# Optimization experiments

Hardware: AMD Instinct MI355X
Metric: run time of the kernel (lower is better)

Reference implementation:

```python
import jax, jax.numpy as jnp
import numpy as np

DIM = 1024
N_HEADS = 16
HEAD_DIM = DIM // N_HEADS
MLP_RATIO = 4
LN_EPS = 1e-5


def _layer_norm(x, w):
    xf = x.astype(jnp.float32)
    mu = jnp.mean(xf, axis=-1, keepdims=True)
    var = jnp.var(xf, axis=-1, keepdims=True)
    y = (xf - mu) / jnp.sqrt(var + LN_EPS)
    return y * w[None, None, :]


def _apply_rope(x, cos, sin):
    # x: (b, s, h, d); cos, sin: (s, d/2)
    c = jnp.concatenate([cos, cos], axis=-1)[None, :, None, :]  # (1,s,1,d)
    s_ = jnp.concatenate([sin, sin], axis=-1)[None, :, None, :]
    x1, x2 = jnp.split(x, 2, axis=-1)
    rot = jnp.concatenate([-x2, x1], axis=-1)
    return x * c + rot * s_


def setup_inputs() -> dict:
    key = jax.random.key(0)
    ks = jax.random.split(key, 12)
    b, s = 2, 2048
    x = jax.random.normal(ks[0], (b, s, DIM), dtype=jnp.float32)
    rot_cos = jax.random.uniform(ks[1], (1, s, 1, 1, HEAD_DIM), dtype=jnp.float32)
    rot_sin = jax.random.uniform(ks[2], (1, s, 1, 1, HEAD_DIM), dtype=jnp.float32)
    w_init = 0.02
    params = {
        'ln1_w': jnp.ones((DIM,), jnp.float32),
        'w_qkv': jax.random.normal(ks[3], (3 * DIM, DIM), jnp.float32) * w_init,
        'w_out': jax.random.normal(ks[4], (DIM, DIM), jnp.float32) * w_init,
        'ln2_w': jnp.ones((DIM,), jnp.float32),
        'w_mlp1': jax.random.normal(ks[5], (MLP_RATIO * DIM, DIM), jnp.float32) * w_init,
        'b_mlp1': jnp.zeros((MLP_RATIO * DIM,), jnp.float32),
        'w_mlp2': jax.random.normal(ks[6], (DIM, MLP_RATIO * DIM), jnp.float32) * w_init,
        'b_mlp2': jnp.zeros((DIM,), jnp.float32),
    }
    return {'x': x, 'rot_cos': rot_cos, 'rot_sin': rot_sin, **params}


def reference(x, rot_cos, rot_sin, ln1_w, w_qkv, w_out, ln2_w, w_mlp1, b_mlp1, w_mlp2, b_mlp2):
    b, s, _ = x.shape
    # _split_rotary: (1,s,1,1,hd) -> (s, hd/2)
    cos = rot_cos[0, :, 0, 0, : HEAD_DIM // 2]
    sin = rot_sin[0, :, 0, 0, : HEAD_DIM // 2]

    x_skip = x
    h1 = _layer_norm(x, ln1_w)
    qkv = jnp.einsum('bsd,ed->bse', h1, w_qkv).reshape(b, s, 3, N_HEADS, HEAD_DIM)
    q, k, v = qkv[:, :, 0], qkv[:, :, 1], qkv[:, :, 2]
    q = _apply_rope(q, cos, sin)
    k = _apply_rope(k, cos, sin)

    # causal SDPA, scale = 1/sqrt(head_dim) (flex_attention default)
    scale = 1.0 / np.sqrt(HEAD_DIM)
    scores = jnp.einsum('bqhd,bkhd->bhqk', q, k) * scale
    causal = jnp.tril(jnp.ones((s, s), dtype=bool))
    scores = jnp.where(causal[None, None], scores, -jnp.inf)
    attn = jax.nn.softmax(scores, axis=-1)
    o = jnp.einsum('bhqk,bkhd->bqhd', attn, v).reshape(b, s, DIM)

    # attn out + residual (eval: dropout off, scale=1)
    x = x_skip + jnp.einsum('bsd,ed->bse', o, w_out)

    # MLP with tanh GELU + residual
    h2 = _layer_norm(x, ln2_w)
    u = jnp.einsum('bsd,ed->bse', h2, w_mlp1) + b_mlp1
    u = jax.nn.gelu(u, approximate=True)
    m = jnp.einsum('bse,de->bsd', u, w_mlp2) + b_mlp2
    return x + m
```

## Files before the change

kernel.cpp:

```cpp
#include <hip/hip_runtime.h>
#include <hip/hip_bf16.h>
#include <math.h>


#define B_ 2
#define S_ 2048
#define D_ 1024
#define H_ 16
#define DH_ 64
#define MLP_ 4096
#define ROWS_ (B_ * S_)

typedef short bf16x8 __attribute__((ext_vector_type(8)));
typedef float f32x4 __attribute__((ext_vector_type(4)));
typedef unsigned short ushort_t;
typedef ushort_t u16x4 __attribute__((ext_vector_type(4)));
typedef unsigned int u32x2 __attribute__((ext_vector_type(2)));

__device__ __forceinline__ float wave_reduce_sum(float v) {
  #pragma unroll
  for (int off = 32; off > 0; off >>= 1) v += __shfl_down(v, off, 64);
  return v;
}

__device__ __forceinline__ ushort_t f2bf(float v) {
  __hip_bfloat16 h = __float2bfloat16(v);
  return *(ushort_t*)&h;
}
__device__ __forceinline__ float bf2f(ushort_t u) {
  unsigned int v = ((unsigned int)u) << 16;
  union { unsigned int i; float f; } c; c.i = v; return c.f;
}

__device__ __forceinline__ void async_copy16(const void* g, void* l) {
  __builtin_amdgcn_global_load_lds(
      (const __attribute__((address_space(1))) void*)g,
      (__attribute__((address_space(3))) void*)l, 16, 0, 0);
}

__global__ __launch_bounds__(256) void cast_w_kernel(
    const float* __restrict__ s0, ushort_t* __restrict__ d0, int n0,
    const float* __restrict__ s1, ushort_t* __restrict__ d1, int n1,
    const float* __restrict__ s2, ushort_t* __restrict__ d2, int n2,
    const float* __restrict__ s3, ushort_t* __restrict__ d3, int n3) {
  const float* s; ushort_t* d; int n;
  switch (blockIdx.y) {
    case 0: s = s0; d = d0; n = n0; break;
    case 1: s = s1; d = d1; n = n1; break;
    case 2: s = s2; d = d2; n = n2; break;
    default: s = s3; d = d3; n = n3; break;
  }
  const int i = (blockIdx.x * 256 + threadIdx.x) * 4;
  if (i < n) {
    const float4 v = *reinterpret_cast<const float4*>(s + i);
    u16x4 o;
    o[0] = f2bf(v.x); o[1] = f2bf(v.y); o[2] = f2bf(v.z); o[3] = f2bf(v.w);
    *reinterpret_cast<u16x4*>(d + i) = o;
  }
}

__global__ __launch_bounds__(256) void ln_kernel(
    const float* __restrict__ x, const float* __restrict__ w,
    ushort_t* __restrict__ y) {
  const int row = blockIdx.x;
  const float4 v = reinterpret_cast<const float4*>(x + (size_t)row * D_)[threadIdx.x];
  float s  = v.x + v.y + v.z + v.w;
  float ss = v.x * v.x + v.y * v.y + v.z * v.z + v.w * v.w;
  __shared__ float red[8];
  const int wave = threadIdx.x >> 6, lane = threadIdx.x & 63;
  const float ws1 = wave_reduce_sum(s);
  const float ws2 = wave_reduce_sum(ss);
  if (lane == 0) { red[wave] = ws1; red[4 + wave] = ws2; }
  __syncthreads();
  const float tot  = red[0] + red[1] + red[2] + red[3];
  const float tot2 = red[4] + red[5] + red[6] + red[7];
  const float mu  = tot * (1.0f / D_);
  const float var = tot2 * (1.0f / D_) - mu * mu;
  const float inv = rsqrtf(var + 1e-5f);
  const float4 wv = reinterpret_cast<const float4*>(w)[threadIdx.x];
  u16x4 o;
  o[0] = f2bf((v.x - mu) * inv * wv.x);
  o[1] = f2bf((v.y - mu) * inv * wv.y);
  o[2] = f2bf((v.z - mu) * inv * wv.z);
  o[3] = f2bf((v.w - mu) * inv * wv.w);
  reinterpret_cast<u16x4*>(y + (size_t)row * D_)[threadIdx.x] = o;
}

__device__ __forceinline__ float gelu_tanh(float u) {
  const float u3 = u * u * u;
  const float t = tanhf(0.7978845608028654f * (u + 0.044715f * u3));
  return 0.5f * u * (1.0f + t);
}

template <int FUSE, int OUTBF, int QKV>
__global__ __launch_bounds__(256) void gemm_bt(
    const ushort_t* __restrict__ A, const ushort_t* __restrict__ W,
    const float* __restrict__ bias, const float* __restrict__ res,
    void* __restrict__ Cv, ushort_t* __restrict__ VtOut,
    int M, int N, int K, int sm, int sn, int rects_n) {
  __shared__ ushort_t As[2][128 * 32];
  __shared__ ushort_t Bs[2][128 * 32];
  const int tid = threadIdx.x;
  const int wave = tid >> 6, lane = tid & 63;
  const int l15 = lane & 15, quad = lane >> 4;

  const int lin = blockIdx.x;
  const int xcd = lin & 7, j = lin >> 3;
  const int rm = xcd / rects_n, rn = xcd % rects_n;
  const int m0 = (rm * sm + (j % sm)) * 128;
  const int n0 = (rn * sn + (j / sm)) * 128;
  const int wm = (wave & 1) * 64, wn = (wave >> 1) * 64;

  const int srow = tid >> 2;
  const int gcol = (((tid & 3) ^ (srow & 3)) * 8);
  const ushort_t* Ag = A + (size_t)(m0 + srow) * K + gcol;
  const ushort_t* Wg = W + (size_t)(n0 + srow) * K + gcol;

  f32x4 acc[4][4] = {};
  const int rslot = (quad ^ (l15 & 3)) * 8;

  const int NI = K >> 5;
  async_copy16(Ag,          &As[0][tid * 8]);
  async_copy16(Ag + 64 * K, &As[0][2048 + tid * 8]);
  async_copy16(Wg,          &Bs[0][tid * 8]);
  async_copy16(Wg + 64 * K, &Bs[0][2048 + tid * 8]);

  for (int i = 0; i < NI; ++i) {
    const int st = i & 1;
    __syncthreads();
    if (i + 1 < NI) {
      const int k1 = (i + 1) << 5;
      async_copy16(Ag + k1,          &As[1 - st][tid * 8]);
      async_copy16(Ag + 64 * K + k1, &As[1 - st][2048 + tid * 8]);
      async_copy16(Wg + k1,          &Bs[1 - st][tid * 8]);
      async_copy16(Wg + 64 * K + k1, &Bs[1 - st][2048 + tid * 8]);
    }
    bf16x8 af[4], bfr[4];
    #pragma unroll
    for (int ii = 0; ii < 4; ++ii) {
      af[ii]  = *(const bf16x8*)&As[st][(wm + ii * 16 + l15) * 32 + rslot];
      bfr[ii] = *(const bf16x8*)&Bs[st][(wn + ii * 16 + l15) * 32 + rslot];
    }
    #pragma unroll
    for (int ii = 0; ii < 4; ++ii)
      #pragma unroll
      for (int jj = 0; jj < 4; ++jj)
        acc[ii][jj] = __builtin_amdgcn_mfma_f32_16x16x32_bf16(af[ii], bfr[jj], acc[ii][jj], 0, 0, 0);
  }

  #pragma unroll
  for (int i = 0; i < 4; ++i) {
    const int mb = m0 + wm + i * 16 + quad * 4;
    #pragma unroll
    for (int jj = 0; jj < 4; ++jj) {
      const int n = n0 + wn + jj * 16 + l15;
      float cv[4];
      #pragma unroll
      for (int r = 0; r < 4; ++r) {
        float c = acc[i][jj][r];
        if (FUSE & 1) c += bias[n];
        if (FUSE & 2) c = gelu_tanh(c);
        if (FUSE & 4) c += res[(size_t)(mb + r) * N + n];
        cv[r] = c;
      }
      if (QKV && ((n0 + wn) >> 10) == 2) {
        const int d  = n & 63;
        const int hh = (n >> 6) & 15;
        const int bb = mb >> 11;
        const int ss = mb & (S_ - 1);
        u16x4 pk;
        #pragma unroll
        for (int r = 0; r < 4; ++r) pk[r] = f2bf(cv[r]);
        *(u16x4*)&VtOut[((size_t)(bb * H_ + hh) * DH_ + d) * S_ + ss] = pk;
      } else {
        #pragma unroll
        for (int r = 0; r < 4; ++r) {
          if (OUTBF) ((ushort_t*)Cv)[(size_t)(mb + r) * N + n] = f2bf(cv[r]);
          else       ((float*)Cv)[(size_t)(mb + r) * N + n]   = cv[r];
        }
      }
    }
  }
}

template <int FUSE, int OUTBF>
__global__ __launch_bounds__(256) void gemm64_bt(
    const ushort_t* __restrict__ A, const ushort_t* __restrict__ W,
    const float* __restrict__ bias, const float* __restrict__ res,
    void* __restrict__ Cv, int M, int N, int K, int sm, int sn, int rects_n) {
  __shared__ ushort_t As[2][64 * 64];
  __shared__ ushort_t Bs[2][128 * 64];
  const int tid = threadIdx.x;
  const int wave = tid >> 6, lane = tid & 63;
  const int l15 = lane & 15, quad = lane >> 4;

  const int lin = blockIdx.x;
  const int xcd = lin & 7, j = lin >> 3;
  const int rm = xcd / rects_n, rn = xcd % rects_n;
  const int m0 = (rm * sm + (j % sm)) * 64;
  const int n0 = (rn * sn + (j / sm)) * 128;
  const int wn = wave * 32;

  const int srow = tid >> 3;
  const int gcol = (((tid & 7) ^ (srow & 7)) * 8);
  const ushort_t* Ag = A + (size_t)(m0 + srow) * K + gcol;
  const ushort_t* Wg = W + (size_t)(n0 + srow) * K + gcol;

  f32x4 acc[4][2] = {};

  const int NI = K >> 6;
  #pragma unroll
  for (int i = 0; i < 2; ++i)
    async_copy16(Ag + (size_t)i * 32 * K, &As[0][i * 2048 + tid * 8]);
  #pragma unroll
  for (int i = 0; i < 4; ++i)
    async_copy16(Wg + (size_t)i * 32 * K, &Bs[0][i * 2048 + tid * 8]);

  for (int it = 0; it < NI; ++it) {
    const int st = it & 1;
    __syncthreads();
    if (it + 1 < NI) {
      const int k1 = (it + 1) << 6;
      #pragma unroll
      for (int i = 0; i < 2; ++i)
        async_copy16(Ag + (size_t)i * 32 * K + k1, &As[1 - st][i * 2048 + tid * 8]);
      #pragma unroll
      for (int i = 0; i < 4; ++i)
        async_copy16(Wg + (size_t)i * 32 * K + k1, &Bs[1 - st][i * 2048 + tid * 8]);
    }
    #pragma unroll
    for (int kk = 0; kk < 2; ++kk) {
      const int slot = (((kk * 4 + quad) ^ (l15 & 7)) * 8);
      bf16x8 af[4], bfr[2];
      #pragma unroll
      for (int i = 0; i < 4; ++i)
        af[i] = *(const bf16x8*)&As[st][(i * 16 + l15) * 64 + slot];
      #pragma unroll
      for (int jj = 0; jj < 2; ++jj)
        bfr[jj] = *(const bf16x8*)&Bs[st][(wn + jj * 16 + l15) * 64 + slot];
      #pragma unroll
      for (int i = 0; i < 4; ++i)
        #pragma unroll
        for (int jj = 0; jj < 2; ++jj)
          acc[i][jj] = __builtin_amdgcn_mfma_f32_16x16x32_bf16(af[i], bfr[jj], acc[i][jj], 0, 0, 0);
    }
  }

  #pragma unroll
  for (int i = 0; i < 4; ++i) {
    const int mb = m0 + i * 16 + quad * 4;
    #pragma unroll
    for (int jj = 0; jj < 2; ++jj) {
      const int n = n0 + wn + jj * 16 + l15;
      #pragma unroll
      for (int r = 0; r < 4; ++r) {
        float c = acc[i][jj][r];
        if (FUSE & 1) c += bias[n];
        if (FUSE & 2) c = gelu_tanh(c);
        if (FUSE & 4) c += res[(size_t)(mb + r) * N + n];
        if (OUTBF) ((ushort_t*)Cv)[(size_t)(mb + r) * N + n] = f2bf(c);
        else       ((float*)Cv)[(size_t)(mb + r) * N + n]   = c;
      }
    }
  }
}

__global__ __launch_bounds__(256) void rope_kernel(
    const ushort_t* __restrict__ qkv, const float* __restrict__ cosb,
    const float* __restrict__ sinb, ushort_t* __restrict__ Qo,
    ushort_t* __restrict__ Ko) {
  const int bs = blockIdx.x;
  const int s  = bs & (S_ - 1);
  const int b  = bs >> 11;
  const int t  = threadIdx.x;
  const ushort_t* base = qkv + (size_t)bs * (3 * D_);
  #pragma unroll
  for (int i = 0; i < 8; ++i) {
    const int e = i * 256 + t;
    const int which = e >> 10;
    const int rem = e & 1023;
    const int h = rem >> 6;
    const int d = rem & 63;
    const float val = bf2f(base[e]);
    float out;
    if (d < 32) {
      out = val * cosb[s * 64 + d] - bf2f(base[e + 32]) * sinb[s * 64 + d];
    } else {
      out = val * cosb[s * 64 + d - 32] + bf2f(base[e - 32]) * sinb[s * 64 + d - 32];
    }
    const size_t oidx = (((size_t)(b * H_ + h)) * S_ + s) * DH_ + d;
    if (which == 0) Qo[oidx] = f2bf(out * 0.125f);
    else            Ko[oidx] = f2bf(out);
  }
}

#define PPAD 72

__global__ __launch_bounds__(256) void attn_kernel(
    const ushort_t* __restrict__ Qb, const ushort_t* __restrict__ Kb,
    const ushort_t* __restrict__ Vt, ushort_t* __restrict__ O) {
  const int wave = threadIdx.x >> 6;
  const int lane = threadIdx.x & 63;
  const int l15 = lane & 15, quad = lane >> 4;
  const int bh = blockIdx.y;
  const int b = bh >> 4, h = bh & 15;
  const int wl = blockIdx.x * 4 + wave;
  const int g  = (wl & 1) ? (63 - (wl >> 1)) : (wl >> 1);
  const int q0 = g * 32;

  __shared__ ushort_t Plds[4][2][16 * PPAD];

  const ushort_t* Kbh = Kb + (size_t)bh * S_ * DH_;
  const ushort_t* Vbh = Vt + (size_t)bh * DH_ * S_;

  bf16x8 qb[2][2];
  #pragma unroll
  for (int t = 0; t < 2; ++t) {
    const ushort_t* qptr = Qb + ((size_t)bh * S_ + q0 + t * 16 + l15) * DH_ + quad * 8;
    qb[t][0] = *(const bf16x8*)(qptr);
    qb[t][1] = *(const bf16x8*)(qptr + 32);
  }

  f32x4 o_acc[2][4] = {};
  float m_run[2] = {-1e30f, -1e30f}, l_run[2] = {0.0f, 0.0f};

  const int nch = (q0 >> 6) + 1;

  bf16x8 ka[4][2];
  #pragma unroll
  for (int kt = 0; kt < 4; ++kt) {
    const ushort_t* kp = Kbh + (size_t)(kt * 16 + l15) * DH_ + quad * 8;
    ka[kt][0] = *(const bf16x8*)kp;
    ka[kt][1] = *(const bf16x8*)(kp + 32);
  }

  for (int c = 0; c < nch; ++c) {
    const int k0 = c << 6;

    bf16x8 va[4][2];
    #pragma unroll
    for (int mt = 0; mt < 4; ++mt) {
      const ushort_t* vp = Vbh + (size_t)(mt * 16 + l15) * S_ + k0 + quad * 8;
      va[mt][0] = *(const bf16x8*)vp;
      va[mt][1] = *(const bf16x8*)(vp + 32);
    }

    f32x4 st[2][4];
    #pragma unroll
    for (int t = 0; t < 2; ++t)
      #pragma unroll
      for (int kt = 0; kt < 4; ++kt) {
        f32x4 z = {0.0f, 0.0f, 0.0f, 0.0f};
        z = __builtin_amdgcn_mfma_f32_16x16x32_bf16(ka[kt][0], qb[t][0], z, 0, 0, 0);
        z = __builtin_amdgcn_mfma_f32_16x16x32_bf16(ka[kt][1], qb[t][1], z, 0, 0, 0);
        st[t][kt] = z;
      }

    if (c + 1 < nch) {
      const int k1 = (c + 1) << 6;
      bf16x8 kan[4][2];
      #pragma unroll
      for (int kt = 0; kt < 4; ++kt) {
        const ushort_t* kp = Kbh + (size_t)(k1 + kt * 16 + l15) * DH_ + quad * 8;
        kan[kt][0] = *(const bf16x8*)kp;
        kan[kt][1] = *(const bf16x8*)(kp + 32);
      }
      #pragma unroll
      for (int kt = 0; kt < 4; ++kt) { ka[kt][0] = kan[kt][0]; ka[kt][1] = kan[kt][1]; }
    }

    if (c == nch - 1) {
      #pragma unroll
      for (int t = 0; t < 2; ++t) {
        const int query = q0 + t * 16 + l15;
        #pragma unroll
        for (int kt = 0; kt < 4; ++kt)
          #pragma unroll
          for (int r = 0; r < 4; ++r)
            if (k0 + kt * 16 + quad * 4 + r > query) st[t][kt][r] = -1e30f;
      }
    }

    #pragma unroll
    for (int t = 0; t < 2; ++t) {
      float mx = -1e30f;
      #pragma unroll
      for (int kt = 0; kt < 4; ++kt)
        #pragma unroll
        for (int r = 0; r < 4; ++r) mx = fmaxf(mx, st[t][kt][r]);
      mx = fmaxf(mx, __shfl_xor(mx, 16, 64));
      mx = fmaxf(mx, __shfl_xor(mx, 32, 64));
      const float m_new = fmaxf(m_run[t], mx);
      const float alpha = __expf(m_run[t] - m_new);
      float rs = 0.0f;
      #pragma unroll
      for (int kt = 0; kt < 4; ++kt)
        #pragma unroll
        for (int r = 0; r < 4; ++r) {
          const float e = __expf(st[t][kt][r] - m_new);
          st[t][kt][r] = e;
          rs += e;
        }
      rs += __shfl_xor(rs, 16, 64);
      rs += __shfl_xor(rs, 32, 64);
      l_run[t] = l_run[t] * alpha + rs;
      m_run[t] = m_new;
      #pragma unroll
      for (int mt = 0; mt < 4; ++mt)
        #pragma unroll
        for (int r = 0; r < 4; ++r) o_acc[t][mt][r] *= alpha;
    }

    #pragma unroll
    for (int t = 0; t < 2; ++t) {
      ushort_t* Pw = &Plds[wave][t][0];
      #pragma unroll
      for (int kt = 0; kt < 4; ++kt) {
        u32x2 wpair;
        wpair[0] = (unsigned)f2bf(st[t][kt][0]) | ((unsigned)f2bf(st[t][kt][1]) << 16);
        wpair[1] = (unsigned)f2bf(st[t][kt][2]) | ((unsigned)f2bf(st[t][kt][3]) << 16);
        *(u32x2*)&Pw[l15 * PPAD + kt * 16 + quad * 4] = wpair;
      }
      asm volatile("s_waitcnt lgkmcnt(0)" ::: "memory");
      const bf16x8 pb0 = *(const bf16x8*)&Pw[l15 * PPAD + quad * 8];
      const bf16x8 pb1 = *(const bf16x8*)&Pw[l15 * PPAD + 32 + quad * 8];
      #pragma unroll
      for (int mt = 0; mt < 4; ++mt) {
        o_acc[t][mt] = __builtin_amdgcn_mfma_f32_16x16x32_bf16(va[mt][0], pb0, o_acc[t][mt], 0, 0, 0);
        o_acc[t][mt] = __builtin_amdgcn_mfma_f32_16x16x32_bf16(va[mt][1], pb1, o_acc[t][mt], 0, 0, 0);
      }
    }
  }

  #pragma unroll
  for (int t = 0; t < 2; ++t) {
    const float inv = 1.0f / l_run[t];
    #pragma unroll
    for (int mt = 0; mt < 4; ++mt) {
      u16x4 pk;
      #pragma unroll
      for (int r = 0; r < 4; ++r) pk[r] = f2bf(o_acc[t][mt][r] * inv);
      *(u16x4*)&O[(((size_t)b * S_ + q0 + t * 16 + l15) * H_ + h) * DH_ + mt * 16 + quad * 4] = pk;
    }
  }
}

extern "C" void kernel_launch(void* const* d_in, const int* in_sizes, int n_in,
                              void* d_out, int out_size, void* d_ws, size_t ws_size,
                              hipStream_t stream) {
  const float* x       = (const float*)d_in[0];
  const float* rot_cos = (const float*)d_in[1];
  const float* rot_sin = (const float*)d_in[2];
  const float* ln1_w   = (const float*)d_in[3];
  const float* w_qkv   = (const float*)d_in[4];
  const float* w_out   = (const float*)d_in[5];
  const float* ln2_w   = (const float*)d_in[6];
  const float* w_mlp1  = (const float*)d_in[7];
  const float* b_mlp1  = (const float*)d_in[8];
  const float* w_mlp2  = (const float*)d_in[9];
  const float* b_mlp2  = (const float*)d_in[10];
  float* out = (float*)d_out;

  char* wsb = (char*)d_ws;
  const size_t MB = 1u << 20;
  ushort_t* h1_bf  = (ushort_t*)(wsb + 0 * MB);
  ushort_t* qkv_bf = (ushort_t*)(wsb + 8 * MB);
  ushort_t* q_bf   = (ushort_t*)(wsb + 32 * MB);
  ushort_t* k_bf   = (ushort_t*)(wsb + 40 * MB);
  ushort_t* v_t    = (ushort_t*)(wsb + 48 * MB);
  ushort_t* o_bf   = (ushort_t*)(wsb + 56 * MB);
  float*    x2     = (float*)   (wsb + 64 * MB);
  ushort_t* u_bf   = (ushort_t*)(wsb + 80 * MB);
  ushort_t* wq_bf  = (ushort_t*)(wsb + 112 * MB);
  ushort_t* wo_bf  = (ushort_t*)(wsb + 118 * MB);
  ushort_t* w1_bf  = (ushort_t*)(wsb + 120 * MB);
  ushort_t* w2_bf  = (ushort_t*)(wsb + 128 * MB);
  (void)ws_size; (void)in_sizes; (void)n_in; (void)out_size;

  dim3 b256(256);

  cast_w_kernel<<<dim3(4096, 4), b256, 0, stream>>>(
      w_qkv, wq_bf, 3 * D_ * D_, w_out, wo_bf, D_ * D_,
      w_mlp1, w1_bf, MLP_ * D_, w_mlp2, w2_bf, MLP_ * D_);
  ln_kernel<<<dim3(ROWS_), b256, 0, stream>>>(x, ln1_w, h1_bf);
  gemm_bt<0, 1, 1><<<dim3(768), b256, 0, stream>>>(
      h1_bf, wq_bf, nullptr, nullptr, qkv_bf, v_t, ROWS_, 3 * D_, D_, 16, 6, 4);
  rope_kernel<<<dim3(ROWS_), b256, 0, stream>>>(qkv_bf, rot_cos, rot_sin, q_bf, k_bf);
  attn_kernel<<<dim3(16, B_ * H_), b256, 0, stream>>>(q_bf, k_bf, v_t, o_bf);
  gemm64_bt<4, 0><<<dim3(512), b256, 0, stream>>>(
      o_bf, wo_bf, nullptr, x, x2, ROWS_, D_, D_, 16, 4, 2);
  ln_kernel<<<dim3(ROWS_), b256, 0, stream>>>(x2, ln2_w, h1_bf);
  gemm_bt<3, 1, 0><<<dim3(1024), b256, 0, stream>>>(
      h1_bf, w1_bf, b_mlp1, nullptr, u_bf, nullptr, ROWS_, MLP_, D_, 16, 8, 4);
  gemm64_bt<5, 0><<<dim3(512), b256, 0, stream>>>(
      u_bf, w2_bf, b_mlp2, x2, out, ROWS_, D_, MLP_, 16, 4, 2);
}
```

Baseline: 386.6 us.

## Split attention waves to 16 queries, use exp2 softmax, retune GEMM LDS swizzle

Each attention wave now handles 16 query rows instead of 32, and the grid doubles so there are twice as many waves, which improves load balance across the causal triangle. The Q scale folds in log2(e) so softmax can use the hardware exp2 instruction instead of __expf. The GEMM LDS XOR swizzle now uses (row>>1)&3 to reduce bank conflicts. The tradeoff is that K/V loads are no longer shared across two query tiles per wave, so each K/V chunk is read twice as often.

```diff
diff --git a/kernel.cpp b/kernel.cpp
--- a/kernel.cpp
+++ b/kernel.cpp
@@ -30,6 +30,14 @@
 __device__ __forceinline__ float bf2f(ushort_t u) {
   unsigned int v = ((unsigned int)u) << 16;
   union { unsigned int i; float f; } c; c.i = v; return c.f;
+}
+
+__device__ __forceinline__ float exp2_fast(float x) {
+#if __has_builtin(__builtin_amdgcn_exp2f)
+  return __builtin_amdgcn_exp2f(x);
+#else
+  return exp2f(x);
+#endif
 }
 
 __device__ __forceinline__ void async_copy16(const void* g, void* l) {
@@ -112,12 +120,12 @@
   const int wm = (wave & 1) * 64, wn = (wave >> 1) * 64;
 
   const int srow = tid >> 2;
-  const int gcol = (((tid & 3) ^ (srow & 3)) * 8);
+  const int gcol = (((tid & 3) ^ ((srow >> 1) & 3)) * 8);
   const ushort_t* Ag = A + (size_t)(m0 + srow) * K + gcol;
   const ushort_t* Wg = W + (size_t)(n0 + srow) * K + gcol;
 
   f32x4 acc[4][4] = {};
-  const int rslot = (quad ^ (l15 & 3)) * 8;
+  const int rslot = (quad ^ ((l15 >> 1) & 3)) * 8;
 
   const int NI = K >> 5;
   async_copy16(Ag,          &As[0][tid * 8]);
@@ -289,7 +297,7 @@
       out = val * cosb[s * 64 + d - 32] + bf2f(base[e - 32]) * sinb[s * 64 + d - 32];
     }
     const size_t oidx = (((size_t)(b * H_ + h)) * S_ + s) * DH_ + d;
-    if (which == 0) Qo[oidx] = f2bf(out * 0.125f);
+    if (which == 0) Qo[oidx] = f2bf(out * 0.18033688736f);
     else            Ko[oidx] = f2bf(out);
   }
 }
@@ -305,24 +313,23 @@
   const int bh = blockIdx.y;
   const int b = bh >> 4, h = bh & 15;
   const int wl = blockIdx.x * 4 + wave;
-  const int g  = (wl & 1) ? (63 - (wl >> 1)) : (wl >> 1);
-  const int q0 = g * 32;
-
-  __shared__ ushort_t Plds[4][2][16 * PPAD];
+  const int g  = (wl & 1) ? (127 - (wl >> 1)) : (wl >> 1);
+  const int q0 = g * 16;
+
+  __shared__ ushort_t Plds[4][16 * PPAD];
 
   const ushort_t* Kbh = Kb + (size_t)bh * S_ * DH_;
   const ushort_t* Vbh = Vt + (size_t)bh * DH_ * S_;
 
-  bf16x8 qb[2][2];
-  #pragma unroll
-  for (int t = 0; t < 2; ++t) {
-    const ushort_t* qptr = Qb + ((size_t)bh * S_ + q0 + t * 16 + l15) * DH_ + quad * 8;
-    qb[t][0] = *(const bf16x8*)(qptr);
-    qb[t][1] = *(const bf16x8*)(qptr + 32);
-  }
-
-  f32x4 o_acc[2][4] = {};
-  float m_run[2] = {-1e30f, -1e30f}, l_run[2] = {0.0f, 0.0f};
+  bf16x8 qb[2];
+  {
+    const ushort_t* qptr = Qb + ((size_t)bh * S_ + q0 + l15) * DH_ + quad * 8;
+    qb[0] = *(const bf16x8*)(qptr);
+    qb[1] = *(const bf16x8*)(qptr + 32);
+  }
+
+  f32x4 o_acc[4] = {};
+  float m_run = -1e30f, l_run = 0.0f;
 
   const int nch = (q0 >> 6) + 1;
 
@@ -345,16 +352,14 @@
       va[mt][1] = *(const bf16x8*)(vp + 32);
     }
 
-    f32x4 st[2][4];
-    #pragma unroll
-    for (int t = 0; t < 2; ++t)
-      #pragma unroll
-      for (int kt = 0; kt < 4; ++kt) {
-        f32x4 z = {0.0f, 0.0f, 0.0f, 0.0f};
-        z = __builtin_amdgcn_mfma_f32_16x16x32_bf16(ka[kt][0], qb[t][0], z, 0, 0, 0);
-        z = __builtin_amdgcn_mfma_f32_16x16x32_bf16(ka[kt][1], qb[t][1], z, 0, 0, 0);
-        st[t][kt] = z;
-      }
+    f32x4 st[4];
+    #pragma unroll
+    for (int kt = 0; kt < 4; ++kt) {
+      f32x4 z = {0.0f, 0.0f, 0.0f, 0.0f};
+      z = __builtin_amdgcn_mfma_f32_16x16x32_bf16(ka[kt][0], qb[0], z, 0, 0, 0);
+      z = __builtin_amdgcn_mfma_f32_16x16x32_bf16(ka[kt][1], qb[1], z, 0, 0, 0);
+      st[kt] = z;
+    }
 
     if (c + 1 < nch) {
       const int k1 = (c + 1) << 6;
@@ -370,55 +375,50 @@
     }
 
     if (c == nch - 1) {
-      #pragma unroll
-      for (int t = 0; t < 2; ++t) {
-        const int query = q0 + t * 16 + l15;
-        #pragma unroll
-        for (int kt = 0; kt < 4; ++kt)
-          #pragma unroll
-          for (int r = 0; r < 4; ++r)
-            if (k0 + kt * 16 + quad * 4 + r > query) st[t][kt][r] = -1e30f;
-      }
-    }
-
-    #pragma unroll
-    for (int t = 0; t < 2; ++t) {
+      const int query = q0 + l15;
+      #pragma unroll
+      for (int kt = 0; kt < 4; ++kt)
+        #pragma unroll
+        for (int r = 0; r < 4; ++r)
+          if (k0 + kt * 16 + quad * 4 + r > query) st[kt][r] = -1e30f;
+    }
+
+    {
       float mx = -1e30f;
       #pragma unroll
       for (int kt = 0; kt < 4; ++kt)
         #pragma unroll
-        for (int r = 0; r < 4; ++r) mx = fmaxf(mx, st[t][kt][r]);
+        for (int r = 0; r < 4; ++r) mx = fmaxf(mx, st[kt][r]);
       mx = fmaxf(mx, __shfl_xor(mx, 16, 64));
       mx = fmaxf(mx, __shfl_xor(mx, 32, 64));
-      const float m_new = fmaxf(m_run[t], mx);
-      const float alpha = __expf(m_run[t] - m_new);
+      const float m_new = fmaxf(m_run, mx);
+      const float alpha = exp2_fast(m_run - m_new);
       float rs = 0.0f;
       #pragma unroll
       for (int kt = 0; kt < 4; ++kt)
         #pragma unroll
         for (int r = 0; r < 4; ++r) {
-          const float e = __expf(st[t][kt][r] - m_new);
-          st[t][kt][r] = e;
+          const float e = exp2_fast(st[kt][r] - m_new);
+          st[kt][r] = e;
           rs += e;
         }
       rs += __shfl_xor(rs, 16, 64);
       rs += __shfl_xor(rs, 32, 64);
-      l_run[t] = l_run[t] * alpha + rs;
-      m_run[t] = m_new;
+      l_run = l_run * alpha + rs;
+      m_run = m_new;
       #pragma unroll
       for (int mt = 0; mt < 4; ++mt)
         #pragma unroll
-        for (int r = 0; r < 4; ++r) o_acc[t][mt][r] *= alpha;
-    }
-
-    #pragma unroll
-    for (int t = 0; t < 2; ++t) {
-      ushort_t* Pw = &Plds[wave][t][0];
+        for (int r = 0; r < 4; ++r) o_acc[mt][r] *= alpha;
+    }
+
+    {
+      ushort_t* Pw = &Plds[wave][0];
       #pragma unroll
       for (int kt = 0; kt < 4; ++kt) {
         u32x2 wpair;
-        wpair[0] = (unsigned)f2bf(st[t][kt][0]) | ((unsigned)f2bf(st[t][kt][1]) << 16);
-        wpair[1] = (unsigned)f2bf(st[t][kt][2]) | ((unsigned)f2bf(st[t][kt][3]) << 16);
+        wpair[0] = (unsigned)f2bf(st[kt][0]) | ((unsigned)f2bf(st[kt][1]) << 16);
+        wpair[1] = (unsigned)f2bf(st[kt][2]) | ((unsigned)f2bf(st[kt][3]) << 16);
         *(u32x2*)&Pw[l15 * PPAD + kt * 16 + quad * 4] = wpair;
       }
       asm volatile("s_waitcnt lgkmcnt(0)" ::: "memory");
@@ -426,21 +426,20 @@
       const bf16x8 pb1 = *(const bf16x8*)&Pw[l15 * PPAD + 32 + quad * 8];
       #pragma unroll
       for (int mt = 0; mt < 4; ++mt) {
-        o_acc[t][mt] = __builtin_amdgcn_mfma_f32_16x16x32_bf16(va[mt][0], pb0, o_acc[t][mt], 0, 0, 0);
-        o_acc[t][mt] = __builtin_amdgcn_mfma_f32_16x16x32_bf16(va[mt][1], pb1, o_acc[t][mt], 0, 0, 0);
-      }
-    }
-  }
-
-  #pragma unroll
-  for (int t = 0; t < 2; ++t) {
-    const float inv = 1.0f / l_run[t];
+        o_acc[mt] = __builtin_amdgcn_mfma_f32_16x16x32_bf16(va[mt][0], pb0, o_acc[mt], 0, 0, 0);
+        o_acc[mt] = __builtin_amdgcn_mfma_f32_16x16x32_bf16(va[mt][1], pb1, o_acc[mt], 0, 0, 0);
+      }
+    }
+  }
+
+  {
+    const float inv = 1.0f / l_run;
     #pragma unroll
     for (int mt = 0; mt < 4; ++mt) {
       u16x4 pk;
       #pragma unroll
-      for (int r = 0; r < 4; ++r) pk[r] = f2bf(o_acc[t][mt][r] * inv);
-      *(u16x4*)&O[(((size_t)b * S_ + q0 + t * 16 + l15) * H_ + h) * DH_ + mt * 16 + quad * 4] = pk;
+      for (int r = 0; r < 4; ++r) pk[r] = f2bf(o_acc[mt][r] * inv);
+      *(u16x4*)&O[(((size_t)b * S_ + q0 + l15) * H_ + h) * DH_ + mt * 16 + quad * 4] = pk;
     }
   }
 }
@@ -486,7 +485,7 @@
   gemm_bt<0, 1, 1><<<dim3(768), b256, 0, stream>>>(
       h1_bf, wq_bf, nullptr, nullptr, qkv_bf, v_t, ROWS_, 3 * D_, D_, 16, 6, 4);
   rope_kernel<<<dim3(ROWS_), b256, 0, stream>>>(qkv_bf, rot_cos, rot_sin, q_bf, k_bf);
-  attn_kernel<<<dim3(16, B_ * H_), b256, 0, stream>>>(q_bf, k_bf, v_t, o_bf);
+  attn_kernel<<<dim3(32, B_ * H_), b256, 0, stream>>>(q_bf, k_bf, v_t, o_bf);
   gemm64_bt<4, 0><<<dim3(512), b256, 0, stream>>>(
       o_bf, wo_bf, nullptr, x, x2, ROWS_, D_, D_, 16, 4, 2);
   ln_kernel<<<dim3(ROWS_), b256, 0, stream>>>(x2, ln2_w, h1_bf);
```

Result: slower. 452.7 us (+17.1%).

## Split attention KV range across two waves with combine kernel, use exp2 softmax

Applied to the files above, without the earlier changes.

Each query tile's causal KV chunks are split into two halves processed by separate waves, which write unnormalized fp32 partial outputs plus running max and sum. A new combine kernel merges the two halves and writes bf16 output. The aim is more parallelism and better load balance for the attention stage. The change also folds log2(e) into the Q scale so softmax can use exp2, changes the GEMM LDS swizzle pattern, and adds s_setprio around the MFMA blocks. The cost is extra fp32 partial-output traffic and an additional kernel launch.

```diff
diff --git a/kernel.cpp b/kernel.cpp
--- a/kernel.cpp
+++ b/kernel.cpp
@@ -30,6 +30,14 @@
 __device__ __forceinline__ float bf2f(ushort_t u) {
   unsigned int v = ((unsigned int)u) << 16;
   union { unsigned int i; float f; } c; c.i = v; return c.f;
+}
+
+__device__ __forceinline__ float exp2_fast(float x) {
+#if __has_builtin(__builtin_amdgcn_exp2f)
+  return __builtin_amdgcn_exp2f(x);
+#else
+  return exp2f(x);
+#endif
 }
 
 __device__ __forceinline__ void async_copy16(const void* g, void* l) {
@@ -112,12 +120,12 @@
   const int wm = (wave & 1) * 64, wn = (wave >> 1) * 64;
 
   const int srow = tid >> 2;
-  const int gcol = (((tid & 3) ^ (srow & 3)) * 8);
+  const int gcol = (((tid & 3) ^ ((srow >> 1) & 3)) * 8);
   const ushort_t* Ag = A + (size_t)(m0 + srow) * K + gcol;
   const ushort_t* Wg = W + (size_t)(n0 + srow) * K + gcol;
 
   f32x4 acc[4][4] = {};
-  const int rslot = (quad ^ (l15 & 3)) * 8;
+  const int rslot = (quad ^ ((l15 >> 1) & 3)) * 8;
 
   const int NI = K >> 5;
   async_copy16(Ag,          &As[0][tid * 8]);
@@ -289,7 +297,7 @@
       out = val * cosb[s * 64 + d - 32] + bf2f(base[e - 32]) * sinb[s * 64 + d - 32];
     }
     const size_t oidx = (((size_t)(b * H_ + h)) * S_ + s) * DH_ + d;
-    if (which == 0) Qo[oidx] = f2bf(out * 0.125f);
+    if (which == 0) Qo[oidx] = f2bf(out * 0.18033688736f);
     else            Ko[oidx] = f2bf(out);
   }
 }
@@ -298,17 +306,43 @@
 
 __global__ __launch_bounds__(256) void attn_kernel(
     const ushort_t* __restrict__ Qb, const ushort_t* __restrict__ Kb,
-    const ushort_t* __restrict__ Vt, ushort_t* __restrict__ O) {
+    const ushort_t* __restrict__ Vt, float* __restrict__ Opart,
+    float2* __restrict__ MLpart) {
   const int wave = threadIdx.x >> 6;
   const int lane = threadIdx.x & 63;
   const int l15 = lane & 15, quad = lane >> 4;
   const int bh = blockIdx.y;
-  const int b = bh >> 4, h = bh & 15;
   const int wl = blockIdx.x * 4 + wave;
-  const int g  = (wl & 1) ? (63 - (wl >> 1)) : (wl >> 1);
+  const int j  = wl >> 1, half = wl & 1;
+  const int g  = (j & 1) ? (63 - (j >> 1)) : (j >> 1);
   const int q0 = g * 32;
 
   __shared__ ushort_t Plds[4][2][16 * PPAD];
+
+  const int nch   = (q0 >> 6) + 1;
+  const int c_mid = (nch + 1) >> 1;
+  const int c_lo  = half ? c_mid : 0;
+  const int c_hi  = half ? nch : c_mid;
+
+  float*  Obase  = Opart + (size_t)half * ((size_t)B_ * H_ * S_ * DH_)
+                 + ((size_t)bh * S_ + q0) * DH_;
+  float2* MLbase = MLpart + (size_t)half * ((size_t)B_ * H_ * S_)
+                 + (size_t)bh * S_ + q0;
+
+  if (c_lo >= c_hi) {
+    const f32x4 z = {0.0f, 0.0f, 0.0f, 0.0f};
+    #pragma unroll
+    for (int t = 0; t < 2; ++t)
+      #pragma unroll
+      for (int mt = 0; mt < 4; ++mt)
+        *(f32x4*)&Obase[(size_t)(t * 16 + l15) * DH_ + mt * 16 + quad * 4] = z;
+    if (quad == 0) {
+      #pragma unroll
+      for (int t = 0; t < 2; ++t)
+        MLbase[t * 16 + l15] = make_float2(-1e30f, 0.0f);
+    }
+    return;
+  }
 
   const ushort_t* Kbh = Kb + (size_t)bh * S_ * DH_;
   const ushort_t* Vbh = Vt + (size_t)bh * DH_ * S_;
@@ -324,17 +358,15 @@
   f32x4 o_acc[2][4] = {};
   float m_run[2] = {-1e30f, -1e30f}, l_run[2] = {0.0f, 0.0f};
 
-  const int nch = (q0 >> 6) + 1;
-
   bf16x8 ka[4][2];
   #pragma unroll
   for (int kt = 0; kt < 4; ++kt) {
-    const ushort_t* kp = Kbh + (size_t)(kt * 16 + l15) * DH_ + quad * 8;
+    const ushort_t* kp = Kbh + (size_t)(c_lo * 64 + kt * 16 + l15) * DH_ + quad * 8;
     ka[kt][0] = *(const bf16x8*)kp;
     ka[kt][1] = *(const bf16x8*)(kp + 32);
   }
 
-  for (int c = 0; c < nch; ++c) {
+  for (int c = c_lo; c < c_hi; ++c) {
     const int k0 = c << 6;
 
     bf16x8 va[4][2];
@@ -346,6 +378,7 @@
     }
 
     f32x4 st[2][4];
+    __builtin_amdgcn_s_setprio(1);
     #pragma unroll
     for (int t = 0; t < 2; ++t)
       #pragma unroll
@@ -355,8 +388,9 @@
         z = __builtin_amdgcn_mfma_f32_16x16x32_bf16(ka[kt][1], qb[t][1], z, 0, 0, 0);
         st[t][kt] = z;
       }
-
-    if (c + 1 < nch) {
+    __builtin_amdgcn_s_setprio(0);
+
+    if (c + 1 < c_hi) {
       const int k1 = (c + 1) << 6;
       bf16x8 kan[4][2];
       #pragma unroll
@@ -391,13 +425,13 @@
       mx = fmaxf(mx, __shfl_xor(mx, 16, 64));
       mx = fmaxf(mx, __shfl_xor(mx, 32, 64));
       const float m_new = fmaxf(m_run[t], mx);
-      const float alpha = __expf(m_run[t] - m_new);
+      const float alpha = exp2_fast(m_run[t] - m_new);
       float rs = 0.0f;
       #pragma unroll
       for (int kt = 0; kt < 4; ++kt)
         #pragma unroll
         for (int r = 0; r < 4; ++r) {
-          const float e = __expf(st[t][kt][r] - m_new);
+          const float e = exp2_fast(st[t][kt][r] - m_new);
           st[t][kt][r] = e;
           rs += e;
         }
@@ -424,25 +458,47 @@
       asm volatile("s_waitcnt lgkmcnt(0)" ::: "memory");
       const bf16x8 pb0 = *(const bf16x8*)&Pw[l15 * PPAD + quad * 8];
       const bf16x8 pb1 = *(const bf16x8*)&Pw[l15 * PPAD + 32 + quad * 8];
+      __builtin_amdgcn_s_setprio(1);
       #pragma unroll
       for (int mt = 0; mt < 4; ++mt) {
         o_acc[t][mt] = __builtin_amdgcn_mfma_f32_16x16x32_bf16(va[mt][0], pb0, o_acc[t][mt], 0, 0, 0);
         o_acc[t][mt] = __builtin_amdgcn_mfma_f32_16x16x32_bf16(va[mt][1], pb1, o_acc[t][mt], 0, 0, 0);
       }
+      __builtin_amdgcn_s_setprio(0);
     }
   }
 
   #pragma unroll
   for (int t = 0; t < 2; ++t) {
-    const float inv = 1.0f / l_run[t];
-    #pragma unroll
-    for (int mt = 0; mt < 4; ++mt) {
-      u16x4 pk;
-      #pragma unroll
-      for (int r = 0; r < 4; ++r) pk[r] = f2bf(o_acc[t][mt][r] * inv);
-      *(u16x4*)&O[(((size_t)b * S_ + q0 + t * 16 + l15) * H_ + h) * DH_ + mt * 16 + quad * 4] = pk;
-    }
-  }
+    #pragma unroll
+    for (int mt = 0; mt < 4; ++mt)
+      *(f32x4*)&Obase[(size_t)(t * 16 + l15) * DH_ + mt * 16 + quad * 4] = o_acc[t][mt];
+    if (quad == 0) MLbase[t * 16 + l15] = make_float2(m_run[t], l_run[t]);
+  }
+}
+
+__global__ __launch_bounds__(256) void attn_combine(
+    const float* __restrict__ Opart, const float2* __restrict__ MLpart,
+    ushort_t* __restrict__ O) {
+  const int tid = threadIdx.x;
+  const int row = blockIdx.x * 16 + (tid >> 4);
+  const int d0  = (tid & 15) * 4;
+  const size_t HALF_O  = (size_t)B_ * H_ * S_ * DH_;
+  const size_t HALF_ML = (size_t)B_ * H_ * S_;
+  const f32x4 o1 = *(const f32x4*)&Opart[(size_t)row * DH_ + d0];
+  const f32x4 o2 = *(const f32x4*)&Opart[HALF_O + (size_t)row * DH_ + d0];
+  const float2 ml1 = MLpart[row];
+  const float2 ml2 = MLpart[HALF_ML + row];
+  const float m  = fmaxf(ml1.x, ml2.x);
+  const float e1 = exp2_fast(ml1.x - m);
+  const float e2 = exp2_fast(ml2.x - m);
+  const float inv = 1.0f / (ml1.y * e1 + ml2.y * e2);
+  const int bh = row >> 11, q = row & (S_ - 1);
+  const int b = bh >> 4, h = bh & 15;
+  u16x4 pk;
+  #pragma unroll
+  for (int r = 0; r < 4; ++r) pk[r] = f2bf((o1[r] * e1 + o2[r] * e2) * inv);
+  *(u16x4*)&O[(((size_t)b * S_ + q) * H_ + h) * DH_ + d0] = pk;
 }
 
 extern "C" void kernel_launch(void* const* d_in, const int* in_sizes, int n_in,
@@ -471,10 +527,12 @@
   ushort_t* o_bf   = (ushort_t*)(wsb + 56 * MB);
   float*    x2     = (float*)   (wsb + 64 * MB);
   ushort_t* u_bf   = (ushort_t*)(wsb + 80 * MB);
+  float*    opart  = (float*)   (wsb + 80 * MB);
   ushort_t* wq_bf  = (ushort_t*)(wsb + 112 * MB);
   ushort_t* wo_bf  = (ushort_t*)(wsb + 118 * MB);
   ushort_t* w1_bf  = (ushort_t*)(wsb + 120 * MB);
   ushort_t* w2_bf  = (ushort_t*)(wsb + 128 * MB);
+  float2*   mlpart = (float2*)  (wsb + 136 * MB);
   (void)ws_size; (void)in_sizes; (void)n_in; (void)out_size;
 
   dim3 b256(256);
@@ -486,7 +544,8 @@
   gemm_bt<0, 1, 1><<<dim3(768), b256, 0, stream>>>(
       h1_bf, wq_bf, nullptr, nullptr, qkv_bf, v_t, ROWS_, 3 * D_, D_, 16, 6, 4);
   rope_kernel<<<dim3(ROWS_), b256, 0, stream>>>(qkv_bf, rot_cos, rot_sin, q_bf, k_bf);
-  attn_kernel<<<dim3(16, B_ * H_), b256, 0, stream>>>(q_bf, k_bf, v_t, o_bf);
+  attn_kernel<<<dim3(32, B_ * H_), b256, 0, stream>>>(q_bf, k_bf, v_t, opart, mlpart);
+  attn_combine<<<dim3(4096), b256, 0, stream>>>(opart, mlpart, o_bf);
   gemm64_bt<4, 0><<<dim3(512), b256, 0, stream>>>(
       o_bf, wo_bf, nullptr, x, x2, ROWS_, D_, D_, 16, 4, 2);
   ln_kernel<<<dim3(ROWS_), b256, 0, stream>>>(x2, ln2_w, h1_bf);
```

After: 396.6 us. 1.03x slower.

## Share K/V tiles in LDS across waves in attention and use exp2 softmax

Applied to the files above, without the earlier changes.

The attention kernel now has each block cover 128 consecutive queries (4 waves × 32) and stage K and V chunks into double-buffered, XOR-swizzled LDS with async global-to-LDS copies, so the four waves share one load instead of each fetching K/V from global memory. Block order is heaviest-first for load balance. The Q scale now folds in log2(e) so softmax can use the hardware exp2, and MFMA sections are wrapped in s_setprio. The GEMM LDS swizzle also changes to use row>>1 bits. The cost is that waves with shorter causal ranges sit idle at block barriers.

```diff
diff --git a/kernel.cpp b/kernel.cpp
--- a/kernel.cpp
+++ b/kernel.cpp
@@ -30,6 +30,14 @@
 __device__ __forceinline__ float bf2f(ushort_t u) {
   unsigned int v = ((unsigned int)u) << 16;
   union { unsigned int i; float f; } c; c.i = v; return c.f;
+}
+
+__device__ __forceinline__ float exp2_fast(float x) {
+#if __has_builtin(__builtin_amdgcn_exp2f)
+  return __builtin_amdgcn_exp2f(x);
+#else
+  return exp2f(x);
+#endif
 }
 
 __device__ __forceinline__ void async_copy16(const void* g, void* l) {
@@ -112,12 +120,12 @@
   const int wm = (wave & 1) * 64, wn = (wave >> 1) * 64;
 
   const int srow = tid >> 2;
-  const int gcol = (((tid & 3) ^ (srow & 3)) * 8);
+  const int gcol = (((tid & 3) ^ ((srow >> 1) & 3)) * 8);
   const ushort_t* Ag = A + (size_t)(m0 + srow) * K + gcol;
   const ushort_t* Wg = W + (size_t)(n0 + srow) * K + gcol;
 
   f32x4 acc[4][4] = {};
-  const int rslot = (quad ^ (l15 & 3)) * 8;
+  const int rslot = (quad ^ ((l15 >> 1) & 3)) * 8;
 
   const int NI = K >> 5;
   async_copy16(Ag,          &As[0][tid * 8]);
@@ -289,7 +297,7 @@
       out = val * cosb[s * 64 + d - 32] + bf2f(base[e - 32]) * sinb[s * 64 + d - 32];
     }
     const size_t oidx = (((size_t)(b * H_ + h)) * S_ + s) * DH_ + d;
-    if (which == 0) Qo[oidx] = f2bf(out * 0.125f);
+    if (which == 0) Qo[oidx] = f2bf(out * 0.18033688736f);
     else            Ko[oidx] = f2bf(out);
   }
 }
@@ -299,19 +307,39 @@
 __global__ __launch_bounds__(256) void attn_kernel(
     const ushort_t* __restrict__ Qb, const ushort_t* __restrict__ Kb,
     const ushort_t* __restrict__ Vt, ushort_t* __restrict__ O) {
-  const int wave = threadIdx.x >> 6;
-  const int lane = threadIdx.x & 63;
+  __shared__ ushort_t Ks[2][64 * 64];
+  __shared__ ushort_t Vs[2][64 * 64];
+  __shared__ ushort_t Plds[4][2][16 * PPAD];
+
+  const int tid  = threadIdx.x;
+  const int wave = tid >> 6;
+  const int lane = tid & 63;
   const int l15 = lane & 15, quad = lane >> 4;
-  const int bh = blockIdx.y;
+
+  const int lin = blockIdx.x;
+  const int bh  = lin & 31;
+  const int g   = 15 - (lin >> 5);
   const int b = bh >> 4, h = bh & 15;
-  const int wl = blockIdx.x * 4 + wave;
-  const int g  = (wl & 1) ? (63 - (wl >> 1)) : (wl >> 1);
-  const int q0 = g * 32;
-
-  __shared__ ushort_t Plds[4][2][16 * PPAD];
+  const int q0 = g * 128 + wave * 32;
+
+  const int nch_w   = (q0 >> 6) + 1;
+  const int nch_max = 2 * g + 2;
 
   const ushort_t* Kbh = Kb + (size_t)bh * S_ * DH_;
   const ushort_t* Vbh = Vt + (size_t)bh * DH_ * S_;
+
+  auto stage = [&](int buf, int c) {
+    const int k0s = c << 6;
+    #pragma unroll
+    for (int i = 0; i < 2; ++i) {
+      const int idx  = i * 256 + tid;
+      const int row  = idx >> 3;
+      const int slot = idx & 7;
+      const int scol = ((slot ^ (row & 7)) * 8);
+      async_copy16(Kbh + (size_t)(k0s + row) * DH_ + scol, &Ks[buf][idx * 8]);
+      async_copy16(Vbh + (size_t)row * S_ + k0s + scol,    &Vs[buf][idx * 8]);
+    }
+  };
 
   bf16x8 qb[2][2];
   #pragma unroll
@@ -324,28 +352,26 @@
   f32x4 o_acc[2][4] = {};
   float m_run[2] = {-1e30f, -1e30f}, l_run[2] = {0.0f, 0.0f};
 
-  const int nch = (q0 >> 6) + 1;
-
-  bf16x8 ka[4][2];
-  #pragma unroll
-  for (int kt = 0; kt < 4; ++kt) {
-    const ushort_t* kp = Kbh + (size_t)(kt * 16 + l15) * DH_ + quad * 8;
-    ka[kt][0] = *(const bf16x8*)kp;
-    ka[kt][1] = *(const bf16x8*)(kp + 32);
-  }
-
-  for (int c = 0; c < nch; ++c) {
+  stage(0, 0);
+
+  for (int c = 0; c < nch_max; ++c) {
+    const int st = c & 1;
+    __syncthreads();
+    if (c + 1 < nch_max) stage(st ^ 1, c + 1);
+    if (c >= nch_w) continue;
     const int k0 = c << 6;
 
-    bf16x8 va[4][2];
-    #pragma unroll
-    for (int mt = 0; mt < 4; ++mt) {
-      const ushort_t* vp = Vbh + (size_t)(mt * 16 + l15) * S_ + k0 + quad * 8;
-      va[mt][0] = *(const bf16x8*)vp;
-      va[mt][1] = *(const bf16x8*)(vp + 32);
-    }
-
-    f32x4 st[2][4];
+    bf16x8 ka[4][2];
+    #pragma unroll
+    for (int kt = 0; kt < 4; ++kt) {
+      const int row = kt * 16 + l15;
+      const int bse = row * 64, rx = row & 7;
+      ka[kt][0] = *(const bf16x8*)&Ks[st][bse + ((quad ^ rx) * 8)];
+      ka[kt][1] = *(const bf16x8*)&Ks[st][bse + (((4 + quad) ^ rx) * 8)];
+    }
+
+    f32x4 s_t[2][4];
+    __builtin_amdgcn_s_setprio(1);
     #pragma unroll
     for (int t = 0; t < 2; ++t)
       #pragma unroll
@@ -353,23 +379,11 @@
         f32x4 z = {0.0f, 0.0f, 0.0f, 0.0f};
         z = __builtin_amdgcn_mfma_f32_16x16x32_bf16(ka[kt][0], qb[t][0], z, 0, 0, 0);
         z = __builtin_amdgcn_mfma_f32_16x16x32_bf16(ka[kt][1], qb[t][1], z, 0, 0, 0);
-        st[t][kt] = z;
-      }
-
-    if (c + 1 < nch) {
-      const int k1 = (c + 1) << 6;
-      bf16x8 kan[4][2];
-      #pragma unroll
-      for (int kt = 0; kt < 4; ++kt) {
-        const ushort_t* kp = Kbh + (size_t)(k1 + kt * 16 + l15) * DH_ + quad * 8;
-        kan[kt][0] = *(const bf16x8*)kp;
-        kan[kt][1] = *(const bf16x8*)(kp + 32);
-      }
-      #pragma unroll
-      for (int kt = 0; kt < 4; ++kt) { ka[kt][0] = kan[kt][0]; ka[kt][1] = kan[kt][1]; }
-    }
-
-    if (c == nch - 1) {
+        s_t[t][kt] = z;
+      }
+    __builtin_amdgcn_s_setprio(0);
+
+    if (c == nch_w - 1) {
       #pragma unroll
       for (int t = 0; t < 2; ++t) {
         const int query = q0 + t * 16 + l15;
@@ -377,7 +391,7 @@
         for (int kt = 0; kt < 4; ++kt)
           #pragma unroll
           for (int r = 0; r < 4; ++r)
-            if (k0 + kt * 16 + quad * 4 + r > query) st[t][kt][r] = -1e30f;
+            if (k0 + kt * 16 + quad * 4 + r > query) s_t[t][kt][r] = -1e30f;
       }
     }
 
@@ -387,18 +401,18 @@
       #pragma unroll
       for (int kt = 0; kt < 4; ++kt)
         #pragma unroll
-        for (int r = 0; r < 4; ++r) mx = fmaxf(mx, st[t][kt][r]);
+        for (int r = 0; r < 4; ++r) mx = fmaxf(mx, s_t[t][kt][r]);
       mx = fmaxf(mx, __shfl_xor(mx, 16, 64));
       mx = fmaxf(mx, __shfl_xor(mx, 32, 64));
       const float m_new = fmaxf(m_run[t], mx);
-      const float alpha = __expf(m_run[t] - m_new);
+      const float alpha = exp2_fast(m_run[t] - m_new);
       float rs = 0.0f;
       #pragma unroll
       for (int kt = 0; kt < 4; ++kt)
         #pragma unroll
         for (int r = 0; r < 4; ++r) {
-          const float e = __expf(st[t][kt][r] - m_new);
-          st[t][kt][r] = e;
+          const float e = exp2_fast(s_t[t][kt][r] - m_new);
+          s_t[t][kt][r] = e;
           rs += e;
         }
       rs += __shfl_xor(rs, 16, 64);
@@ -411,24 +425,35 @@
         for (int r = 0; r < 4; ++r) o_acc[t][mt][r] *= alpha;
     }
 
+    bf16x8 va[4][2];
+    #pragma unroll
+    for (int mt = 0; mt < 4; ++mt) {
+      const int row = mt * 16 + l15;
+      const int bse = row * 64, rx = row & 7;
+      va[mt][0] = *(const bf16x8*)&Vs[st][bse + ((quad ^ rx) * 8)];
+      va[mt][1] = *(const bf16x8*)&Vs[st][bse + (((4 + quad) ^ rx) * 8)];
+    }
+
     #pragma unroll
     for (int t = 0; t < 2; ++t) {
       ushort_t* Pw = &Plds[wave][t][0];
       #pragma unroll
       for (int kt = 0; kt < 4; ++kt) {
         u32x2 wpair;
-        wpair[0] = (unsigned)f2bf(st[t][kt][0]) | ((unsigned)f2bf(st[t][kt][1]) << 16);
-        wpair[1] = (unsigned)f2bf(st[t][kt][2]) | ((unsigned)f2bf(st[t][kt][3]) << 16);
+        wpair[0] = (unsigned)f2bf(s_t[t][kt][0]) | ((unsigned)f2bf(s_t[t][kt][1]) << 16);
+        wpair[1] = (unsigned)f2bf(s_t[t][kt][2]) | ((unsigned)f2bf(s_t[t][kt][3]) << 16);
         *(u32x2*)&Pw[l15 * PPAD + kt * 16 + quad * 4] = wpair;
       }
       asm volatile("s_waitcnt lgkmcnt(0)" ::: "memory");
       const bf16x8 pb0 = *(const bf16x8*)&Pw[l15 * PPAD + quad * 8];
       const bf16x8 pb1 = *(const bf16x8*)&Pw[l15 * PPAD + 32 + quad * 8];
+      __builtin_amdgcn_s_setprio(1);
       #pragma unroll
       for (int mt = 0; mt < 4; ++mt) {
         o_acc[t][mt] = __builtin_amdgcn_mfma_f32_16x16x32_bf16(va[mt][0], pb0, o_acc[t][mt], 0, 0, 0);
         o_acc[t][mt] = __builtin_amdgcn_mfma_f32_16x16x32_bf16(va[mt][1], pb1, o_acc[t][mt], 0, 0, 0);
       }
+      __builtin_amdgcn_s_setprio(0);
     }
   }
 
@@ -486,7 +511,7 @@
   gemm_bt<0, 1, 1><<<dim3(768), b256, 0, stream>>>(
       h1_bf, wq_bf, nullptr, nullptr, qkv_bf, v_t, ROWS_, 3 * D_, D_, 16, 6, 4);
   rope_kernel<<<dim3(ROWS_), b256, 0, stream>>>(qkv_bf, rot_cos, rot_sin, q_bf, k_bf);
-  attn_kernel<<<dim3(16, B_ * H_), b256, 0, stream>>>(q_bf, k_bf, v_t, o_bf);
+  attn_kernel<<<dim3(512), b256, 0, stream>>>(q_bf, k_bf, v_t, o_bf);
   gemm64_bt<4, 0><<<dim3(512), b256, 0, stream>>>(
       o_bf, wo_bf, nullptr, x, x2, ROWS_, D_, D_, 16, 4, 2);
   ln_kernel<<<dim3(ROWS_), b256, 0, stream>>>(x2, ln2_w, h1_bf);
```

Result: faster. 376.6 us (-2.6%).
